# Performance work log

Measured on AMD Instinct MI355X. Metric: run time of the kernel, lower is better.

## Reference

```python
import jax, jax.numpy as jnp
import numpy as np

LOGIT_SCALE = 1.0
REDUCTION = "mean"

N, H, V = 4096, 512, 50257


def setup_inputs() -> dict:
    key = jax.random.key(0)
    k1, k2, k3, k4 = jax.random.split(key, 4)
    x = jax.random.normal(k1, (N, H), dtype=jnp.float32)
    targets = jax.random.normal(k2, (N, V), dtype=jnp.float32)
    weight = jax.random.normal(k3, (V, H), dtype=jnp.float32) * 0.02
    bias = jax.random.normal(k4, (V,), dtype=jnp.float32) * 0.02
    return {"x": x, "targets": targets, "weight": weight, "bias": bias}


def reference(x, targets, weight, bias):
    # logits = x @ W^T + b  -> [N, V]
    logits = jnp.einsum("nh,vh->nv", x, weight) + bias
    scaled = logits * LOGIT_SCALE
    # logsumexp over vocab for both predicted and target logits (fp32)
    lse_logits = jax.nn.logsumexp(scaled, axis=-1)                      # [N]
    lse_targets = jax.nn.logsumexp(targets, axis=-1)                    # [N]
    # original: .nan_to_num(nan=inf) -> rows with nan targets contribute 0
    lse_targets = jnp.where(jnp.isnan(lse_targets), jnp.inf, lse_targets)
    p_target = jnp.exp(targets - lse_targets[:, None])                  # softmax(targets)
    log_p_pred = scaled - lse_logits[:, None]                           # log_softmax(scaled logits)
    per_row_loss = -jnp.sum(p_target * log_p_pred, axis=-1)             # [N]
    loss = per_row_loss.sum()
    if REDUCTION == "mean":
        loss = loss / N
    return loss
```

## Files before the change

### kernel.cpp

```cpp
#include <hip/hip_runtime.h>
#include <hip/hip_bf16.h>

#define N_ROWS 4096
#define H_DIM  512
#define V_DIM  50257
#define BM 128
#define BN 128
#define BK 64
#define NSTEP (H_DIM / BK)
#define VT_TOTAL 393
#define V_PAD (VT_TOTAL * BN)
#define NCHUNK 131
#define LOG2E 1.4426950408889634f
#define BUF0 0
#define BUF1 32768
#define LBASE 32768

#define VMCNT8() asm volatile("s_waitcnt vmcnt(8)" ::: "memory")
#define VMCNT0() asm volatile("s_waitcnt vmcnt(0)" ::: "memory")
#define LGKM0()  asm volatile("s_waitcnt lgkmcnt(0)" ::: "memory")
#define BARRIER() __builtin_amdgcn_s_barrier()

typedef __attribute__((ext_vector_type(8))) short short8;
typedef __attribute__((ext_vector_type(4))) float f32x4;

static __device__ __forceinline__ unsigned short f2bf(float f) {
  unsigned u = __float_as_uint(f);
  u = (u + 0x7fffu + ((u >> 16) & 1u)) >> 16;
  return (unsigned short)u;
}

static __device__ __forceinline__ void gload_lds16(const void* g, void* l) {
  __builtin_amdgcn_global_load_lds(
      (const __attribute__((address_space(1))) void*)g,
      (__attribute__((address_space(3))) void*)l, 16, 0, 0);
}

__global__ void convert_kernel(const float* __restrict__ X,
                               const float* __restrict__ W,
                               __hip_bfloat16* __restrict__ Xb,
                               __hip_bfloat16* __restrict__ Wb) {
  const long wtot8 = (long)V_PAD * H_DIM / 8;
  const long xtot8 = (long)N_ROWS * H_DIM / 8;
  long i = (long)blockIdx.x * blockDim.x + threadIdx.x;
  unsigned short o[8];
  if (i < wtot8) {
    long base = i * 8;
    long row = base >> 9;
    if (row < V_DIM) {
      const float4* s = (const float4*)(W + base);
      float4 a = s[0], b = s[1];
      o[0]=f2bf(a.x); o[1]=f2bf(a.y); o[2]=f2bf(a.z); o[3]=f2bf(a.w);
      o[4]=f2bf(b.x); o[5]=f2bf(b.y); o[6]=f2bf(b.z); o[7]=f2bf(b.w);
    } else {
      #pragma unroll
      for (int k = 0; k < 8; ++k) o[k] = 0;
    }
    *(short8*)(Wb + base) = *(const short8*)o;
  } else if (i < wtot8 + xtot8) {
    long base = (i - wtot8) * 8;
    const float4* s = (const float4*)(X + base);
    float4 a = s[0], b = s[1];
    o[0]=f2bf(a.x); o[1]=f2bf(a.y); o[2]=f2bf(a.z); o[3]=f2bf(a.w);
    o[4]=f2bf(b.x); o[5]=f2bf(b.y); o[6]=f2bf(b.z); o[7]=f2bf(b.w);
    *(short8*)(Xb + base) = *(const short8*)o;
  }
}

template <bool GUARD>
static __device__ __forceinline__ void chunk_stats(
    const float (&Lraw)[16], const f32x4 (&T)[4], int gcol0,
    float& mlr, float& slr, float& mtr, float& str, float& ddr) {
  float Lv[16], Tv[16];
  #pragma unroll
  for (int k = 0; k < 16; ++k) {
    const bool ok = !GUARD || (gcol0 + k < V_DIM);
    Lv[k] = ok ? Lraw[k] : -1e30f;
    Tv[k] = ok ? T[k >> 2][k & 3] : -1e30f;
  }
  float g = Lv[0];
  #pragma unroll
  for (int k = 1; k < 16; ++k) g = fmaxf(g, Lv[k]);
  if (g > mlr + 12.f) { slr *= exp2f((mlr - g) * LOG2E); mlr = g; }
  float bl = mlr * LOG2E;
  float ss = 0.f;
  #pragma unroll
  for (int k = 0; k < 16; ++k) ss += exp2f(__builtin_fmaf(Lv[k], LOG2E, -bl));
  slr += ss;
  float gt = Tv[0];
  #pragma unroll
  for (int k = 1; k < 16; ++k) gt = fmaxf(gt, Tv[k]);
  if (gt > mtr + 12.f) {
    float sc = exp2f((mtr - gt) * LOG2E);
    str *= sc; ddr *= sc; mtr = gt;
  }
  float bt = mtr * LOG2E;
  float s2 = 0.f, d2 = 0.f;
  #pragma unroll
  for (int k = 0; k < 16; ++k) {
    float e = exp2f(__builtin_fmaf(Tv[k], LOG2E, -bt));
    s2 += e;
    d2 = __builtin_fmaf(e, Lv[k], d2);
  }
  str += s2; ddr += d2;
}

template <bool GUARD>
static __device__ __forceinline__ void stream_tile(
    const float* __restrict__ targets, const char* __restrict__ Lrow,
    long growVD, int vbase, int cb0, int rsw, long tlim,
    float& mlr, float& slr, float& mtr, float& str, float& ddr) {
  f32x4 T0[4], T1[4];
  auto LOADT = [&](f32x4 (&D)[4], int i) {
    #pragma unroll
    for (int c = 0; c < 4; ++c) {
      long off = growVD + vbase + cb0 + i * 16 + c * 4;
      if (GUARD) off = off > tlim ? tlim : off;
      D[c] = *(const f32x4*)(targets + off);
    }
  };
  auto DOCHUNK = [&](const f32x4 (&T)[4], int i) {
    const int ob = (cb0 << 1) + (i << 5);
    short8 l0 = *(const short8*)(Lrow + ((ob) ^ rsw));
    short8 l1 = *(const short8*)(Lrow + ((ob + 16) ^ rsw));
    float Lraw[16];
    #pragma unroll
    for (int e = 0; e < 8; ++e) {
      Lraw[e]     = __uint_as_float(((unsigned)(unsigned short)l0[e]) << 16);
      Lraw[e + 8] = __uint_as_float(((unsigned)(unsigned short)l1[e]) << 16);
    }
    chunk_stats<GUARD>(Lraw, T, vbase + cb0 + i * 16, mlr, slr, mtr, str, ddr);
  };
  LOADT(T0, 0); LOADT(T1, 1);
  DOCHUNK(T0, 0);
  LOADT(T0, 2);
  DOCHUNK(T1, 1);
  LOADT(T1, 3);
  DOCHUNK(T0, 2);
  DOCHUNK(T1, 3);
}

__global__ __launch_bounds__(256, 2)
void fused_kernel(const __hip_bfloat16* __restrict__ Xb,
                  const __hip_bfloat16* __restrict__ Wb,
                  const float* __restrict__ bias,
                  const float* __restrict__ targets,
                  float* __restrict__ partials) {
  __shared__ __align__(16) char smem[65536];

  const int tid  = threadIdx.x;
  const int lane = tid & 63;
  const int wid  = tid >> 6;
  const int wm   = wid >> 1;
  const int wn   = wid & 1;
  const int q    = lane >> 4;
  const int c15  = lane & 15;
  const int brow = blockIdx.x;
  const int chunk = blockIdx.y;

  float mlr = -1e30f, slr = 0.f, mtr = -1e30f, str = 0.f, ddr = 0.f;

  const int srow8 = tid >> 3;
  const int soff  = ((tid & 7) * 8) ^ ((srow8 & 7) * 8);
  const __hip_bfloat16* asrc = Xb + (long)(brow * BM + srow8) * H_DIM + soff;

  const int rm      = (c15 & 7) << 4;
  const int arow_b  = (wm * 64 + c15) * 128;
  const int brow_b  = (wn * 64 + c15) * 128;

  auto stage = [&](int bufb, const __hip_bfloat16* a_s,
                   const __hip_bfloat16* b_s, int kk) {
    #pragma unroll
    for (int i = 0; i < 4; ++i)
      gload_lds16(a_s + (long)i * 32 * H_DIM + kk,
                  smem + bufb + i * 4096 + tid * 16);
    #pragma unroll
    for (int i = 0; i < 4; ++i)
      gload_lds16(b_s + (long)i * 32 * H_DIM + kk,
                  smem + bufb + 16384 + i * 4096 + tid * 16);
  };

  const int srow  = tid >> 1;
  const int shalf = tid & 1;
  const int cb0   = shalf * 64;
  const long grow   = (long)(brow * BM + srow);
  const long growVD = grow * V_DIM;
  const long tlim   = (long)N_ROWS * V_DIM - 4;
  const char* Lrow  = smem + LBASE + srow * 256;
  const int rsw     = (srow & 7) << 4;

  const __hip_bfloat16* bsrc = Wb + (long)(chunk * BN + srow8) * H_DIM + soff;
  stage(BUF0, asrc, bsrc, 0);

  #pragma unroll 1
  for (int vt = chunk; vt < VT_TOTAL; vt += NCHUNK) {
    const int vbase = vt * BN;
    const int v0 = vbase + wn * 64 + q * 4;
    const bool last = (vt + NCHUNK >= VT_TOTAL);
    const __hip_bfloat16* bsrc_next =
        Wb + (long)((vt + NCHUNK) * BN + srow8) * H_DIM + soff;

    f32x4 acc[4][4];
    #pragma unroll
    for (int a = 0; a < 4; ++a)
      #pragma unroll
      for (int b = 0; b < 4; ++b)
        acc[a][b] = (f32x4){0.f, 0.f, 0.f, 0.f};

    #pragma unroll
    for (int ks = 0; ks < NSTEP; ++ks) {
      const int cb = (ks & 1) ? BUF1 : BUF0;
      const int nb = cb ^ 32768;
      if (ks < NSTEP - 1)
        stage(nb, asrc, bsrc, (ks + 1) * BK);
      else if (!last)
        stage(nb, asrc, bsrc_next, 0);

      if (ks == NSTEP - 1 && last) { VMCNT0(); } else { VMCNT8(); }
      BARRIER();

      #pragma unroll
      for (int s = 0; s < 2; ++s) {
        short8 xf[4], wf[4];
        #pragma unroll
        for (int a = 0; a < 4; ++a)
          xf[a] = *(const short8*)(smem + cb + arow_b + a * 2048 +
                                   ((s * 64 + q * 16) ^ rm));
        #pragma unroll
        for (int b = 0; b < 4; ++b)
          wf[b] = *(const short8*)(smem + cb + 16384 + brow_b + b * 2048 +
                                   ((s * 64 + q * 16) ^ rm));
        __builtin_amdgcn_s_setprio(1);
        #pragma unroll
        for (int a = 0; a < 4; ++a)
          #pragma unroll
          for (int b = 0; b < 4; ++b)
            acc[a][b] = __builtin_amdgcn_mfma_f32_16x16x32_bf16(
                wf[b], xf[a], acc[a][b], 0, 0, 0);
        __builtin_amdgcn_s_setprio(0);
      }
      LGKM0();
      BARRIER();
    }
    bsrc = bsrc_next;

    f32x4 bp[4];
    #pragma unroll
    for (int b = 0; b < 4; ++b) {
      int bo = v0 + b * 16;
      bo = bo > (V_DIM - 4) ? (V_DIM - 4) : bo;
      bp[b] = *(const f32x4*)(bias + bo);
    }
    #pragma unroll
    for (int a = 0; a < 4; ++a) {
      const int row = wm * 64 + a * 16 + c15;
      char* rb = smem + LBASE + row * 256;
      #pragma unroll
      for (int b = 0; b < 4; ++b) {
        uint2 w;
        w.x = (unsigned)f2bf(acc[a][b][0] + bp[b][0]) |
              ((unsigned)f2bf(acc[a][b][1] + bp[b][1]) << 16);
        w.y = (unsigned)f2bf(acc[a][b][2] + bp[b][2]) |
              ((unsigned)f2bf(acc[a][b][3] + bp[b][3]) << 16);
        const int o = wn * 128 + b * 32 + q * 8;
        *(uint2*)(rb + (o ^ rm)) = w;
      }
    }
    LGKM0();
    BARRIER();

    if (vt == VT_TOTAL - 1)
      stream_tile<true >(targets, Lrow, growVD, vbase, cb0, rsw, tlim,
                         mlr, slr, mtr, str, ddr);
    else
      stream_tile<false>(targets, Lrow, growVD, vbase, cb0, rsw, tlim,
                         mlr, slr, mtr, str, ddr);
    LGKM0();
    BARRIER();
  }

  {
    float ml2 = __shfl_xor(mlr, 1);
    float sl2 = __shfl_xor(slr, 1);
    float mt2 = __shfl_xor(mtr, 1);
    float st2 = __shfl_xor(str, 1);
    float dd2 = __shfl_xor(ddr, 1);
    float nm = fmaxf(mlr, ml2);
    float slo = slr * exp2f((mlr - nm) * LOG2E) + sl2 * exp2f((ml2 - nm) * LOG2E);
    float nmt = fmaxf(mtr, mt2);
    float e1 = exp2f((mtr - nmt) * LOG2E);
    float e2 = exp2f((mt2 - nmt) * LOG2E);
    float sto = str * e1 + st2 * e2;
    float ddo = ddr * e1 + dd2 * e2;
    if (shalf == 0) {
      float* o = partials + (grow * NCHUNK + chunk) * 5;
      o[0] = nm; o[1] = slo; o[2] = nmt; o[3] = sto; o[4] = ddo;
    }
  }
}

__global__ void rowloss_kernel(const float* __restrict__ partials,
                               float* __restrict__ rowloss) {
  int r = blockIdx.x * blockDim.x + threadIdx.x;
  if (r >= N_ROWS) return;
  const float* p = partials + (long)r * NCHUNK * 5;
  float ml = -1e30f, sl = 0.f, mt = -1e30f, st = 0.f, dd = 0.f;
  for (int c = 0; c < NCHUNK; ++c) {
    float ml2 = p[0], sl2 = p[1], mt2 = p[2], st2 = p[3], dd2 = p[4];
    p += 5;
    float nm = fmaxf(ml, ml2);
    sl = sl * exp2f((ml - nm) * LOG2E) + sl2 * exp2f((ml2 - nm) * LOG2E);
    ml = nm;
    float nmt = fmaxf(mt, mt2);
    float e1 = exp2f((mt - nmt) * LOG2E);
    float e2 = exp2f((mt2 - nmt) * LOG2E);
    st = st * e1 + st2 * e2;
    dd = dd * e1 + dd2 * e2;
    mt = nmt;
  }
  float lse = ml + logf(sl);
  rowloss[r] = lse - dd / st;
}

__global__ void final_kernel(const float* __restrict__ rowloss,
                             float* __restrict__ out) {
  __shared__ float sm[4];
  float s = 0.f;
  for (int i = threadIdx.x; i < N_ROWS; i += 256) s += rowloss[i];
  #pragma unroll
  for (int off = 32; off > 0; off >>= 1) s += __shfl_down(s, off);
  if ((threadIdx.x & 63) == 0) sm[threadIdx.x >> 6] = s;
  __syncthreads();
  if (threadIdx.x == 0) out[0] = (sm[0] + sm[1] + sm[2] + sm[3]) * (1.0f / (float)N_ROWS);
}

extern "C" void kernel_launch(void* const* d_in, const int* in_sizes, int n_in,
                              void* d_out, int out_size, void* d_ws, size_t ws_size,
                              hipStream_t stream) {
  const float* x       = (const float*)d_in[0];
  const float* targets = (const float*)d_in[1];
  const float* weight  = (const float*)d_in[2];
  const float* bias    = (const float*)d_in[3];
  float* out = (float*)d_out;

  char* ws = (char*)d_ws;
  __hip_bfloat16* Wb = (__hip_bfloat16*)ws;
  size_t off = (size_t)V_PAD * H_DIM * 2;
  __hip_bfloat16* Xb = (__hip_bfloat16*)(ws + off);
  off += (size_t)N_ROWS * H_DIM * 2;
  float* partials = (float*)(ws + off);
  off += (size_t)N_ROWS * NCHUNK * 5 * sizeof(float);
  float* rowloss = (float*)(ws + off);

  convert_kernel<<<13600, 256, 0, stream>>>(x, weight, Xb, Wb);
  dim3 grid(N_ROWS / BM, NCHUNK);
  fused_kernel<<<grid, 256, 0, stream>>>(Xb, Wb, bias, targets, partials);
  rowloss_kernel<<<N_ROWS / 256, 256, 0, stream>>>(partials, rowloss);
  final_kernel<<<1, 256, 0, stream>>>(rowloss, out);
}
```

Baseline: 558.1 us.

## Prefetch target tile before GEMM, remap blocks across XCDs, drop setprio

The first half of each row's targets slice is loaded into registers before the bf16 MFMA K-loop, and the second half is loaded right after the logits are written to LDS. The aim is to hide the streaming reads of the large targets matrix behind matrix work. The flat block index is also remapped so that consecutive blocks on one XCD share weight chunks, and the s_setprio around the MFMAs is removed. Because vmcnt waits retire loads in order, the early target loads are forced to finish at the first K-step wait, which limits the overlap. Holding 32 extra registers of prefetched targets through the GEMM may also raise register pressure at two waves per SIMD.

Measured after the change: 770.6 us. 38.1% more time.

```diff
diff --git a/kernel.cpp b/kernel.cpp
--- a/kernel.cpp
+++ b/kernel.cpp
@@ -16,9 +16,9 @@
 #define BUF1 32768
 #define LBASE 32768
 
-#define VMCNT8() asm volatile("s_waitcnt vmcnt(8)" ::: "memory")
-#define VMCNT0() asm volatile("s_waitcnt vmcnt(0)" ::: "memory")
 #define LGKM0()  asm volatile("s_waitcnt lgkmcnt(0)" ::: "memory")
+#define VMC0()   asm volatile("s_waitcnt vmcnt(0)" ::: "memory")
+#define VMC8()   asm volatile("s_waitcnt vmcnt(8)" ::: "memory")
 #define BARRIER() __builtin_amdgcn_s_barrier()
 
 typedef __attribute__((ext_vector_type(8))) short short8;
@@ -68,33 +68,33 @@
 }
 
 template <bool GUARD>
-static __device__ __forceinline__ void chunk_stats(
-    const float (&Lraw)[16], const f32x4 (&T)[4], int gcol0,
-    float& mlr, float& slr, float& mtr, float& str, float& ddr) {
+static __device__ __forceinline__ void stats16(
+    const float (&Lraw)[16], const f32x4* T4, int gcol0,
+    float& ml, float& sl, float& mt, float& st, float& dd) {
   float Lv[16], Tv[16];
   #pragma unroll
   for (int k = 0; k < 16; ++k) {
     const bool ok = !GUARD || (gcol0 + k < V_DIM);
     Lv[k] = ok ? Lraw[k] : -1e30f;
-    Tv[k] = ok ? T[k >> 2][k & 3] : -1e30f;
+    Tv[k] = ok ? T4[k >> 2][k & 3] : -1e30f;
   }
   float g = Lv[0];
   #pragma unroll
   for (int k = 1; k < 16; ++k) g = fmaxf(g, Lv[k]);
-  if (g > mlr + 12.f) { slr *= exp2f((mlr - g) * LOG2E); mlr = g; }
-  float bl = mlr * LOG2E;
+  if (g > ml + 12.f) { sl *= exp2f((ml - g) * LOG2E); ml = g; }
+  float bl = ml * LOG2E;
   float ss = 0.f;
   #pragma unroll
   for (int k = 0; k < 16; ++k) ss += exp2f(__builtin_fmaf(Lv[k], LOG2E, -bl));
-  slr += ss;
+  sl += ss;
   float gt = Tv[0];
   #pragma unroll
   for (int k = 1; k < 16; ++k) gt = fmaxf(gt, Tv[k]);
-  if (gt > mtr + 12.f) {
-    float sc = exp2f((mtr - gt) * LOG2E);
-    str *= sc; ddr *= sc; mtr = gt;
-  }
-  float bt = mtr * LOG2E;
+  if (gt > mt + 12.f) {
+    float sc = exp2f((mt - gt) * LOG2E);
+    st *= sc; dd *= sc; mt = gt;
+  }
+  float bt = mt * LOG2E;
   float s2 = 0.f, d2 = 0.f;
   #pragma unroll
   for (int k = 0; k < 16; ++k) {
@@ -102,42 +102,22 @@
     s2 += e;
     d2 = __builtin_fmaf(e, Lv[k], d2);
   }
-  str += s2; ddr += d2;
+  st += s2; dd += d2;
 }
 
 template <bool GUARD>
-static __device__ __forceinline__ void stream_tile(
-    const float* __restrict__ targets, const char* __restrict__ Lrow,
-    long growVD, int vbase, int cb0, int rsw, long tlim,
-    float& mlr, float& slr, float& mtr, float& str, float& ddr) {
-  f32x4 T0[4], T1[4];
-  auto LOADT = [&](f32x4 (&D)[4], int i) {
-    #pragma unroll
-    for (int c = 0; c < 4; ++c) {
-      long off = growVD + vbase + cb0 + i * 16 + c * 4;
-      if (GUARD) off = off > tlim ? tlim : off;
-      D[c] = *(const f32x4*)(targets + off);
-    }
-  };
-  auto DOCHUNK = [&](const f32x4 (&T)[4], int i) {
-    const int ob = (cb0 << 1) + (i << 5);
-    short8 l0 = *(const short8*)(Lrow + ((ob) ^ rsw));
-    short8 l1 = *(const short8*)(Lrow + ((ob + 16) ^ rsw));
-    float Lraw[16];
-    #pragma unroll
-    for (int e = 0; e < 8; ++e) {
-      Lraw[e]     = __uint_as_float(((unsigned)(unsigned short)l0[e]) << 16);
-      Lraw[e + 8] = __uint_as_float(((unsigned)(unsigned short)l1[e]) << 16);
-    }
-    chunk_stats<GUARD>(Lraw, T, vbase + cb0 + i * 16, mlr, slr, mtr, str, ddr);
-  };
-  LOADT(T0, 0); LOADT(T1, 1);
-  DOCHUNK(T0, 0);
-  LOADT(T0, 2);
-  DOCHUNK(T1, 1);
-  LOADT(T1, 3);
-  DOCHUNK(T0, 2);
-  DOCHUNK(T1, 3);
+static __device__ __forceinline__ void dochunk(
+    const f32x4* T4, const char* Lrow, int rsw, int ob, int gc0,
+    float& ml, float& sl, float& mt, float& st, float& dd) {
+  short8 l0 = *(const short8*)(Lrow + (ob ^ rsw));
+  short8 l1 = *(const short8*)(Lrow + ((ob + 16) ^ rsw));
+  float Lraw[16];
+  #pragma unroll
+  for (int e = 0; e < 8; ++e) {
+    Lraw[e]     = __uint_as_float(((unsigned)(unsigned short)l0[e]) << 16);
+    Lraw[e + 8] = __uint_as_float(((unsigned)(unsigned short)l1[e]) << 16);
+  }
+  stats16<GUARD>(Lraw, T4, gc0, ml, sl, mt, st, dd);
 }
 
 __global__ __launch_bounds__(256, 2)
@@ -155,8 +135,11 @@
   const int wn   = wid & 1;
   const int q    = lane >> 4;
   const int c15  = lane & 15;
-  const int brow = blockIdx.x;
-  const int chunk = blockIdx.y;
+
+  int f = blockIdx.y * gridDim.x + blockIdx.x;
+  f = (f & 7) * 524 + (f >> 3);
+  const int brow  = f & 31;
+  const int chunk = f >> 5;
 
   float mlr = -1e30f, slr = 0.f, mtr = -1e30f, str = 0.f, ddr = 0.f;
 
@@ -197,8 +180,17 @@
     const int vbase = vt * BN;
     const int v0 = vbase + wn * 64 + q * 4;
     const bool last = (vt + NCHUNK >= VT_TOTAL);
+    const bool guard = (vt == VT_TOTAL - 1);
     const __hip_bfloat16* bsrc_next =
         Wb + (long)((vt + NCHUNK) * BN + srow8) * H_DIM + soff;
+
+    f32x4 tp0[8];
+    #pragma unroll
+    for (int c = 0; c < 8; ++c) {
+      long off = growVD + vbase + cb0 + c * 4;
+      off = off > tlim ? tlim : off;
+      tp0[c] = *(const f32x4*)(targets + off);
+    }
 
     f32x4 acc[4][4];
     #pragma unroll
@@ -216,7 +208,7 @@
       else if (!last)
         stage(nb, asrc, bsrc_next, 0);
 
-      if (ks == NSTEP - 1 && last) { VMCNT0(); } else { VMCNT8(); }
+      if (ks == NSTEP - 1 && last) { VMC0(); } else { VMC8(); }
       BARRIER();
 
       #pragma unroll
@@ -230,14 +222,12 @@
         for (int b = 0; b < 4; ++b)
           wf[b] = *(const short8*)(smem + cb + 16384 + brow_b + b * 2048 +
                                    ((s * 64 + q * 16) ^ rm));
-        __builtin_amdgcn_s_setprio(1);
         #pragma unroll
         for (int a = 0; a < 4; ++a)
           #pragma unroll
           for (int b = 0; b < 4; ++b)
             acc[a][b] = __builtin_amdgcn_mfma_f32_16x16x32_bf16(
                 wf[b], xf[a], acc[a][b], 0, 0, 0);
-        __builtin_amdgcn_s_setprio(0);
       }
       LGKM0();
       BARRIER();
@@ -269,12 +259,28 @@
     LGKM0();
     BARRIER();
 
-    if (vt == VT_TOTAL - 1)
-      stream_tile<true >(targets, Lrow, growVD, vbase, cb0, rsw, tlim,
-                         mlr, slr, mtr, str, ddr);
-    else
-      stream_tile<false>(targets, Lrow, growVD, vbase, cb0, rsw, tlim,
-                         mlr, slr, mtr, str, ddr);
+    f32x4 tp1[8];
+    #pragma unroll
+    for (int c = 0; c < 8; ++c) {
+      long off = growVD + vbase + cb0 + 32 + c * 4;
+      off = off > tlim ? tlim : off;
+      tp1[c] = *(const f32x4*)(targets + off);
+    }
+    const int ob0 = cb0 * 2;
+    const int gc  = vbase + cb0;
+    if (guard) {
+      dochunk<true >(&tp0[0], Lrow, rsw, ob0,      gc,      mlr, slr, mtr, str, ddr);
+      dochunk<true >(&tp0[4], Lrow, rsw, ob0 + 32, gc + 16, mlr, slr, mtr, str, ddr);
+      VMC0();
+      dochunk<true >(&tp1[0], Lrow, rsw, ob0 + 64, gc + 32, mlr, slr, mtr, str, ddr);
+      dochunk<true >(&tp1[4], Lrow, rsw, ob0 + 96, gc + 48, mlr, slr, mtr, str, ddr);
+    } else {
+      dochunk<false>(&tp0[0], Lrow, rsw, ob0,      gc,      mlr, slr, mtr, str, ddr);
+      dochunk<false>(&tp0[4], Lrow, rsw, ob0 + 32, gc + 16, mlr, slr, mtr, str, ddr);
+      VMC0();
+      dochunk<false>(&tp1[0], Lrow, rsw, ob0 + 64, gc + 32, mlr, slr, mtr, str, ddr);
+      dochunk<false>(&tp1[4], Lrow, rsw, ob0 + 96, gc + 48, mlr, slr, mtr, str, ddr);
+    }
     LGKM0();
     BARRIER();
   }
```

## Switch logits GEMM to FP8 e4m3 MFMA with scaled weights and remapped grid

Applied to the files above, without the earlier changes.

Quantizes X and a 32x-scaled W to FP8 e4m3 in the convert kernel and runs the logits GEMM with fp8 MFMA. The LDS staging layout and swizzle are reworked for byte elements, which halves staging buffers and global loads, and the accumulator is descaled before the bias is added. Block indices are also remapped so consecutive blocks share chunks, for L2 locality, and the setprio hints are removed. This cuts GEMM bandwidth and compute but adds quantization error to the logits, which may break the accuracy tolerance.

Result: slower. 570.0 us (+2.1%).

```diff
diff --git a/kernel.cpp b/kernel.cpp
--- a/kernel.cpp
+++ b/kernel.cpp
@@ -1,5 +1,6 @@
 #include <hip/hip_runtime.h>
 #include <hip/hip_bf16.h>
+#include <hip/hip_fp8.h>
 
 #define N_ROWS 4096
 #define H_DIM  512
@@ -12,12 +13,14 @@
 #define V_PAD (VT_TOTAL * BN)
 #define NCHUNK 131
 #define LOG2E 1.4426950408889634f
+#define WSCALE 32.0f
+#define WDESCALE 0.03125f
 #define BUF0 0
-#define BUF1 32768
+#define BUF1 16384
 #define LBASE 32768
 
-#define VMCNT8() asm volatile("s_waitcnt vmcnt(8)" ::: "memory")
-#define VMCNT0() asm volatile("s_waitcnt vmcnt(0)" ::: "memory")
+#define VMCNT4() asm volatile("s_waitcnt vmcnt(4)" ::: "memory")
+#define VMC0()   asm volatile("s_waitcnt vmcnt(0)" ::: "memory")
 #define LGKM0()  asm volatile("s_waitcnt lgkmcnt(0)" ::: "memory")
 #define BARRIER() __builtin_amdgcn_s_barrier()
 
@@ -30,6 +33,11 @@
   return (unsigned short)u;
 }
 
+static __device__ __forceinline__ unsigned char f2fp8(float f) {
+  __hip_fp8_e4m3 v(f);
+  return (unsigned char)v.__x;
+}
+
 static __device__ __forceinline__ void gload_lds16(const void* g, void* l) {
   __builtin_amdgcn_global_load_lds(
       (const __attribute__((address_space(1))) void*)g,
@@ -38,63 +46,65 @@
 
 __global__ void convert_kernel(const float* __restrict__ X,
                                const float* __restrict__ W,
-                               __hip_bfloat16* __restrict__ Xb,
-                               __hip_bfloat16* __restrict__ Wb) {
+                               unsigned char* __restrict__ Xq,
+                               unsigned char* __restrict__ Wq) {
   const long wtot8 = (long)V_PAD * H_DIM / 8;
   const long xtot8 = (long)N_ROWS * H_DIM / 8;
   long i = (long)blockIdx.x * blockDim.x + threadIdx.x;
-  unsigned short o[8];
+  unsigned char o[8];
   if (i < wtot8) {
     long base = i * 8;
     long row = base >> 9;
     if (row < V_DIM) {
       const float4* s = (const float4*)(W + base);
       float4 a = s[0], b = s[1];
-      o[0]=f2bf(a.x); o[1]=f2bf(a.y); o[2]=f2bf(a.z); o[3]=f2bf(a.w);
-      o[4]=f2bf(b.x); o[5]=f2bf(b.y); o[6]=f2bf(b.z); o[7]=f2bf(b.w);
+      o[0]=f2fp8(WSCALE*a.x); o[1]=f2fp8(WSCALE*a.y);
+      o[2]=f2fp8(WSCALE*a.z); o[3]=f2fp8(WSCALE*a.w);
+      o[4]=f2fp8(WSCALE*b.x); o[5]=f2fp8(WSCALE*b.y);
+      o[6]=f2fp8(WSCALE*b.z); o[7]=f2fp8(WSCALE*b.w);
     } else {
       #pragma unroll
       for (int k = 0; k < 8; ++k) o[k] = 0;
     }
-    *(short8*)(Wb + base) = *(const short8*)o;
+    *(uint2*)(Wq + base) = *(const uint2*)o;
   } else if (i < wtot8 + xtot8) {
     long base = (i - wtot8) * 8;
     const float4* s = (const float4*)(X + base);
     float4 a = s[0], b = s[1];
-    o[0]=f2bf(a.x); o[1]=f2bf(a.y); o[2]=f2bf(a.z); o[3]=f2bf(a.w);
-    o[4]=f2bf(b.x); o[5]=f2bf(b.y); o[6]=f2bf(b.z); o[7]=f2bf(b.w);
-    *(short8*)(Xb + base) = *(const short8*)o;
+    o[0]=f2fp8(a.x); o[1]=f2fp8(a.y); o[2]=f2fp8(a.z); o[3]=f2fp8(a.w);
+    o[4]=f2fp8(b.x); o[5]=f2fp8(b.y); o[6]=f2fp8(b.z); o[7]=f2fp8(b.w);
+    *(uint2*)(Xq + base) = *(const uint2*)o;
   }
 }
 
 template <bool GUARD>
-static __device__ __forceinline__ void chunk_stats(
-    const float (&Lraw)[16], const f32x4 (&T)[4], int gcol0,
-    float& mlr, float& slr, float& mtr, float& str, float& ddr) {
+static __device__ __forceinline__ void stats16(
+    const float (&Lraw)[16], const f32x4* T4, int gcol0,
+    float& ml, float& sl, float& mt, float& st, float& dd) {
   float Lv[16], Tv[16];
   #pragma unroll
   for (int k = 0; k < 16; ++k) {
     const bool ok = !GUARD || (gcol0 + k < V_DIM);
     Lv[k] = ok ? Lraw[k] : -1e30f;
-    Tv[k] = ok ? T[k >> 2][k & 3] : -1e30f;
+    Tv[k] = ok ? T4[k >> 2][k & 3] : -1e30f;
   }
   float g = Lv[0];
   #pragma unroll
   for (int k = 1; k < 16; ++k) g = fmaxf(g, Lv[k]);
-  if (g > mlr + 12.f) { slr *= exp2f((mlr - g) * LOG2E); mlr = g; }
-  float bl = mlr * LOG2E;
+  if (g > ml + 12.f) { sl *= exp2f((ml - g) * LOG2E); ml = g; }
+  float bl = ml * LOG2E;
   float ss = 0.f;
   #pragma unroll
   for (int k = 0; k < 16; ++k) ss += exp2f(__builtin_fmaf(Lv[k], LOG2E, -bl));
-  slr += ss;
+  sl += ss;
   float gt = Tv[0];
   #pragma unroll
   for (int k = 1; k < 16; ++k) gt = fmaxf(gt, Tv[k]);
-  if (gt > mtr + 12.f) {
-    float sc = exp2f((mtr - gt) * LOG2E);
-    str *= sc; ddr *= sc; mtr = gt;
-  }
-  float bt = mtr * LOG2E;
+  if (gt > mt + 12.f) {
+    float sc = exp2f((mt - gt) * LOG2E);
+    st *= sc; dd *= sc; mt = gt;
+  }
+  float bt = mt * LOG2E;
   float s2 = 0.f, d2 = 0.f;
   #pragma unroll
   for (int k = 0; k < 16; ++k) {
@@ -102,7 +112,7 @@
     s2 += e;
     d2 = __builtin_fmaf(e, Lv[k], d2);
   }
-  str += s2; ddr += d2;
+  st += s2; dd += d2;
 }
 
 template <bool GUARD>
@@ -129,7 +139,7 @@
       Lraw[e]     = __uint_as_float(((unsigned)(unsigned short)l0[e]) << 16);
       Lraw[e + 8] = __uint_as_float(((unsigned)(unsigned short)l1[e]) << 16);
     }
-    chunk_stats<GUARD>(Lraw, T, vbase + cb0 + i * 16, mlr, slr, mtr, str, ddr);
+    stats16<GUARD>(Lraw, T, vbase + cb0 + i * 16, mlr, slr, mtr, str, ddr);
   };
   LOADT(T0, 0); LOADT(T1, 1);
   DOCHUNK(T0, 0);
@@ -141,8 +151,8 @@
 }
 
 __global__ __launch_bounds__(256, 2)
-void fused_kernel(const __hip_bfloat16* __restrict__ Xb,
-                  const __hip_bfloat16* __restrict__ Wb,
+void fused_kernel(const unsigned char* __restrict__ Xq,
+                  const unsigned char* __restrict__ Wq,
                   const float* __restrict__ bias,
                   const float* __restrict__ targets,
                   float* __restrict__ partials) {
@@ -155,29 +165,34 @@
   const int wn   = wid & 1;
   const int q    = lane >> 4;
   const int c15  = lane & 15;
-  const int brow = blockIdx.x;
-  const int chunk = blockIdx.y;
+
+  int f = blockIdx.y * gridDim.x + blockIdx.x;
+  f = (f & 7) * 524 + (f >> 3);
+  const int brow  = f & 31;
+  const int chunk = f >> 5;
 
   float mlr = -1e30f, slr = 0.f, mtr = -1e30f, str = 0.f, ddr = 0.f;
 
-  const int srow8 = tid >> 3;
-  const int soff  = ((tid & 7) * 8) ^ ((srow8 & 7) * 8);
-  const __hip_bfloat16* asrc = Xb + (long)(brow * BM + srow8) * H_DIM + soff;
-
-  const int rm      = (c15 & 7) << 4;
-  const int arow_b  = (wm * 64 + c15) * 128;
-  const int brow_b  = (wn * 64 + c15) * 128;
-
-  auto stage = [&](int bufb, const __hip_bfloat16* a_s,
-                   const __hip_bfloat16* b_s, int kk) {
-    #pragma unroll
-    for (int i = 0; i < 4; ++i)
-      gload_lds16(a_s + (long)i * 32 * H_DIM + kk,
+  const int srow4 = tid >> 2;
+  const int soff  = (((tid & 3) ^ (srow4 & 3)) * 16);
+  const unsigned char* asrc = Xq + (long)(brow * BM + srow4) * H_DIM + soff;
+
+  const int rm3    = c15 & 3;
+  const int arow_b = (wm * 64 + c15) * 64;
+  const int brow_b = (wn * 64 + c15) * 64;
+  const int io[2] = { (((q >> 1)) ^ rm3) * 16 + (q & 1) * 8,
+                      ((2 + (q >> 1)) ^ rm3) * 16 + (q & 1) * 8 };
+
+  auto stage = [&](int bufb, const unsigned char* a_s,
+                   const unsigned char* b_s, int kk) {
+    #pragma unroll
+    for (int i = 0; i < 2; ++i)
+      gload_lds16(a_s + (long)i * 64 * H_DIM + kk,
                   smem + bufb + i * 4096 + tid * 16);
     #pragma unroll
-    for (int i = 0; i < 4; ++i)
-      gload_lds16(b_s + (long)i * 32 * H_DIM + kk,
-                  smem + bufb + 16384 + i * 4096 + tid * 16);
+    for (int i = 0; i < 2; ++i)
+      gload_lds16(b_s + (long)i * 64 * H_DIM + kk,
+                  smem + bufb + 8192 + i * 4096 + tid * 16);
   };
 
   const int srow  = tid >> 1;
@@ -189,7 +204,7 @@
   const char* Lrow  = smem + LBASE + srow * 256;
   const int rsw     = (srow & 7) << 4;
 
-  const __hip_bfloat16* bsrc = Wb + (long)(chunk * BN + srow8) * H_DIM + soff;
+  const unsigned char* bsrc = Wq + (long)(chunk * BN + srow4) * H_DIM + soff;
   stage(BUF0, asrc, bsrc, 0);
 
   #pragma unroll 1
@@ -197,8 +212,9 @@
     const int vbase = vt * BN;
     const int v0 = vbase + wn * 64 + q * 4;
     const bool last = (vt + NCHUNK >= VT_TOTAL);
-    const __hip_bfloat16* bsrc_next =
-        Wb + (long)((vt + NCHUNK) * BN + srow8) * H_DIM + soff;
+    const bool guard = (vt == VT_TOTAL - 1);
+    const unsigned char* bsrc_next =
+        Wq + (long)((vt + NCHUNK) * BN + srow4) * H_DIM + soff;
 
     f32x4 acc[4][4];
     #pragma unroll
@@ -210,34 +226,29 @@
     #pragma unroll
     for (int ks = 0; ks < NSTEP; ++ks) {
       const int cb = (ks & 1) ? BUF1 : BUF0;
-      const int nb = cb ^ 32768;
+      const int nb = cb ^ BUF1;
       if (ks < NSTEP - 1)
         stage(nb, asrc, bsrc, (ks + 1) * BK);
       else if (!last)
         stage(nb, asrc, bsrc_next, 0);
-
-      if (ks == NSTEP - 1 && last) { VMCNT0(); } else { VMCNT8(); }
+      if (ks == NSTEP - 1 && last) { VMC0(); } else { VMCNT4(); }
       BARRIER();
 
       #pragma unroll
       for (int s = 0; s < 2; ++s) {
-        short8 xf[4], wf[4];
+        long xf[4], wf[4];
         #pragma unroll
         for (int a = 0; a < 4; ++a)
-          xf[a] = *(const short8*)(smem + cb + arow_b + a * 2048 +
-                                   ((s * 64 + q * 16) ^ rm));
+          xf[a] = *(const long*)(smem + cb + arow_b + a * 1024 + io[s]);
         #pragma unroll
         for (int b = 0; b < 4; ++b)
-          wf[b] = *(const short8*)(smem + cb + 16384 + brow_b + b * 2048 +
-                                   ((s * 64 + q * 16) ^ rm));
-        __builtin_amdgcn_s_setprio(1);
+          wf[b] = *(const long*)(smem + cb + 8192 + brow_b + b * 1024 + io[s]);
         #pragma unroll
         for (int a = 0; a < 4; ++a)
           #pragma unroll
           for (int b = 0; b < 4; ++b)
-            acc[a][b] = __builtin_amdgcn_mfma_f32_16x16x32_bf16(
+            acc[a][b] = __builtin_amdgcn_mfma_f32_16x16x32_fp8_fp8(
                 wf[b], xf[a], acc[a][b], 0, 0, 0);
-        __builtin_amdgcn_s_setprio(0);
       }
       LGKM0();
       BARRIER();
@@ -251,6 +262,7 @@
       bo = bo > (V_DIM - 4) ? (V_DIM - 4) : bo;
       bp[b] = *(const f32x4*)(bias + bo);
     }
+    const int rmL = (c15 & 7) << 4;
     #pragma unroll
     for (int a = 0; a < 4; ++a) {
       const int row = wm * 64 + a * 16 + c15;
@@ -258,18 +270,18 @@
       #pragma unroll
       for (int b = 0; b < 4; ++b) {
         uint2 w;
-        w.x = (unsigned)f2bf(acc[a][b][0] + bp[b][0]) |
-              ((unsigned)f2bf(acc[a][b][1] + bp[b][1]) << 16);
-        w.y = (unsigned)f2bf(acc[a][b][2] + bp[b][2]) |
-              ((unsigned)f2bf(acc[a][b][3] + bp[b][3]) << 16);
+        w.x = (unsigned)f2bf(__builtin_fmaf(acc[a][b][0], WDESCALE, bp[b][0])) |
+              ((unsigned)f2bf(__builtin_fmaf(acc[a][b][1], WDESCALE, bp[b][1])) << 16);
+        w.y = (unsigned)f2bf(__builtin_fmaf(acc[a][b][2], WDESCALE, bp[b][2])) |
+              ((unsigned)f2bf(__builtin_fmaf(acc[a][b][3], WDESCALE, bp[b][3])) << 16);
         const int o = wn * 128 + b * 32 + q * 8;
-        *(uint2*)(rb + (o ^ rm)) = w;
+        *(uint2*)(rb + (o ^ rmL)) = w;
       }
     }
     LGKM0();
     BARRIER();
 
-    if (vt == VT_TOTAL - 1)
+    if (guard)
       stream_tile<true >(targets, Lrow, growVD, vbase, cb0, rsw, tlim,
                          mlr, slr, mtr, str, ddr);
     else
@@ -344,17 +356,18 @@
   float* out = (float*)d_out;
 
   char* ws = (char*)d_ws;
-  __hip_bfloat16* Wb = (__hip_bfloat16*)ws;
-  size_t off = (size_t)V_PAD * H_DIM * 2;
-  __hip_bfloat16* Xb = (__hip_bfloat16*)(ws + off);
-  off += (size_t)N_ROWS * H_DIM * 2;
+  unsigned char* Wq = (unsigned char*)ws;
+  size_t off = (size_t)V_PAD * H_DIM;
+  unsigned char* Xq = (unsigned char*)(ws + off);
+  off += (size_t)N_ROWS * H_DIM;
+  off = (off + 255) & ~(size_t)255;
   float* partials = (float*)(ws + off);
   off += (size_t)N_ROWS * NCHUNK * 5 * sizeof(float);
   float* rowloss = (float*)(ws + off);
 
-  convert_kernel<<<13600, 256, 0, stream>>>(x, weight, Xb, Wb);
+  convert_kernel<<<13600, 256, 0, stream>>>(x, weight, Xq, Wq);
   dim3 grid(N_ROWS / BM, NCHUNK);
-  fused_kernel<<<grid, 256, 0, stream>>>(Xb, Wb, bias, targets, partials);
+  fused_kernel<<<grid, 256, 0, stream>>>(Xq, Wq, bias, targets, partials);
   rowloss_kernel<<<N_ROWS / 256, 256, 0, stream>>>(partials, rowloss);
   final_kernel<<<1, 256, 0, stream>>>(rowloss, out);
 }
```
